# Optimization experiments

Measured on AMD Instinct MI355X. Metric: run time of the kernel, lower is better.

The kernel has to match this reference:

```python
import jax, jax.numpy as jnp
import numpy as np

N_NODES = 100000


def gcn_conv(x, edge_index, W, b):
    """PyG GCNConv: add self-loops, symmetric deg^{-1/2} normalization,
    linear transform, scatter-add aggregation, then bias."""
    n = x.shape[0]
    loops = jnp.arange(n, dtype=edge_index.dtype)
    src = jnp.concatenate([edge_index[0], loops])  # [E+N]
    dst = jnp.concatenate([edge_index[1], loops])  # [E+N]
    # degree (with self-loops) of each target node
    deg = jax.ops.segment_sum(jnp.ones_like(dst, dtype=x.dtype), dst, num_segments=n)
    dinv = jnp.where(deg > 0, jax.lax.rsqrt(deg), 0.0)
    norm = dinv[src] * dinv[dst]  # [E+N]
    h = x @ W  # [N, out_dim] -- transform before aggregation
    msg = h[src] * norm[:, None]  # gather + normalize
    out = jax.ops.segment_sum(msg, dst, num_segments=n)  # scatter-add
    return out + b


def setup_inputs() -> dict:
    key = jax.random.key(0)
    ks = jax.random.split(key, 8)
    n, e, d_in, d_h = N_NODES, 1600000, 32, 64
    x = jax.random.normal(ks[0], (n, d_in), dtype=jnp.float32)
    edge_index = jax.random.randint(ks[1], (2, e), 0, n, dtype=jnp.int64)
    # Glorot-style init for GCN weights, uniform for linear layer
    W1 = jax.random.normal(ks[2], (d_in, d_h), dtype=jnp.float32) / np.sqrt(d_in)
    b1 = jnp.zeros((d_h,), dtype=jnp.float32)
    W2 = jax.random.normal(ks[3], (d_h, d_h), dtype=jnp.float32) / np.sqrt(d_h)
    b2 = jnp.zeros((d_h,), dtype=jnp.float32)
    Wo = jax.random.normal(ks[4], (d_h, 1), dtype=jnp.float32) / np.sqrt(d_h)
    bo = jnp.zeros((1,), dtype=jnp.float32)
    return {"x": x, "edge_index": edge_index, "W1": W1, "b1": b1,
            "W2": W2, "b2": b2, "Wo": Wo, "bo": bo}


def reference(x, edge_index, W1, b1, W2, b2, Wo, bo):
    h = jax.nn.relu(gcn_conv(x, edge_index, W1, b1))
    h = jax.nn.relu(gcn_conv(h, edge_index, W2, b2))
    logits = h @ Wo + bo  # [N, 1]
    return jax.nn.sigmoid(logits).squeeze(-1)  # [N]
```

## Files before the change

kernel.cpp:

```cpp
#include <hip/hip_runtime.h>

#define DH 64
#define DIN 32
#define BSH 8
#define BNODES 256
#define MAXB 1024
#define CAPSH 13
#define CAP (1 << CAPSH)

typedef unsigned short u16;
typedef unsigned int u32;
typedef float f32x2 __attribute__((ext_vector_type(2)));

__device__ __forceinline__ float bf2f(u16 u) {
    union { u32 i; float f; } x; x.i = ((u32)u) << 16; return x.f;
}
__device__ __forceinline__ u16 f2bf(float f) {
    union { float f; u32 i; } x; x.f = f;
    u32 r = x.i + 0x7fff + ((x.i >> 16) & 1);
    return (u16)(r >> 16);
}
__device__ __forceinline__ float bfl(u32 u) {
    union { u32 i; float f; } x; x.i = u << 16; return x.f;
}
__device__ __forceinline__ float bfh(u32 u) {
    union { u32 i; float f; } x; x.i = u & 0xffff0000u; return x.f;
}
__device__ __forceinline__ void pkacc(f32x2& a, u32 u) {
    f32x2 b;
    b[0] = bfl(u); b[1] = bfh(u);
    asm("v_pk_add_f32 %0, %1, %0" : "+v"(a) : "v"(b));
}

__global__ void __launch_bounds__(1024) binA_k(
        const int* __restrict__ ei, int* __restrict__ gcnt,
        u32* __restrict__ pairs, int E, int n, int nbuck) {
    __shared__ int lhist[MAXB];
    __shared__ int lbase[MAXB];
    __shared__ int smode;
    int t = threadIdx.x;
    if (t < 64) {
        int v = (2 * t + 1 < 2 * E) ? ei[2 * t + 1] : 0;
        unsigned long long b = __ballot(v != 0);
        if (t == 0) smode = (b != 0ULL) ? 1 : 0;
    }
    for (int b = t; b < nbuck; b += 1024) lhist[b] = 0;
    __syncthreads();
    int m = smode;
    unsigned un = (unsigned)n;
    int q0 = blockIdx.x * 1024 + t;
    int qs = gridDim.x * 1024;

    if (m && !(E & 3)) {
        const int4* d4 = (const int4*)(ei + E);
        for (int q = q0; q < (E >> 2); q += qs) {
            int4 d = d4[q];
            if ((unsigned)d.x < un) atomicAdd(&lhist[d.x >> BSH], 1);
            if ((unsigned)d.y < un) atomicAdd(&lhist[d.y >> BSH], 1);
            if ((unsigned)d.z < un) atomicAdd(&lhist[d.z >> BSH], 1);
            if ((unsigned)d.w < un) atomicAdd(&lhist[d.w >> BSH], 1);
        }
    } else if (!m && !(E & 1)) {
        const int4* d4 = (const int4*)(ei + 2 * E);
        for (int q = q0; q < (E >> 1); q += qs) {
            int4 d = d4[q];
            if ((unsigned)d.x < un) atomicAdd(&lhist[d.x >> BSH], 1);
            if ((unsigned)d.z < un) atomicAdd(&lhist[d.z >> BSH], 1);
        }
    } else {
        const int* dstp = m ? (ei + E) : (ei + 2 * E);
        int stride = m ? 1 : 2;
        for (int e = q0; e < E; e += qs) {
            int d = dstp[(size_t)e * stride];
            if ((unsigned)d < un) atomicAdd(&lhist[d >> BSH], 1);
        }
    }
    __syncthreads();
    for (int b = t; b < nbuck; b += 1024) {
        int c = lhist[b];
        lbase[b] = c ? ((b << CAPSH) + atomicAdd(&gcnt[b], c)) : 0;
        lhist[b] = 0;
    }
    __syncthreads();
    #define EMIT(S, D)                                                     \
        if ((unsigned)(D) < un) {                                          \
            int sv = ((unsigned)(S) < un) ? (S) : 0;                       \
            int bb = (D) >> BSH;                                           \
            int off = atomicAdd(&lhist[bb], 1);                            \
            int pos = lbase[bb] + off;                                     \
            if (pos < ((bb + 1) << CAPSH))                                 \
                pairs[pos] = ((u32)sv << BSH) | (u32)((D) & (BNODES - 1)); \
        }
    if (m && !(E & 3)) {
        const int4* s4 = (const int4*)ei;
        const int4* d4 = (const int4*)(ei + E);
        for (int q = q0; q < (E >> 2); q += qs) {
            int4 s = s4[q]; int4 d = d4[q];
            EMIT(s.x, d.x) EMIT(s.y, d.y) EMIT(s.z, d.z) EMIT(s.w, d.w)
        }
    } else if (!m && !(E & 1)) {
        const int4* s4 = (const int4*)ei;
        const int4* d4 = (const int4*)(ei + 2 * E);
        for (int q = q0; q < (E >> 1); q += qs) {
            int4 s = s4[q]; int4 d = d4[q];
            EMIT(s.x, d.x) EMIT(s.z, d.z)
        }
    } else {
        const int* srcp = ei;
        const int* dstp = m ? (ei + E) : (ei + 2 * E);
        int stride = m ? 1 : 2;
        for (int e = q0; e < E; e += qs) {
            int d = dstp[(size_t)e * stride];
            int s = srcp[(size_t)e * stride];
            EMIT(s, d)
        }
    }
    #undef EMIT
}

__global__ void __launch_bounds__(1024) csr_build_k(
        const u32* __restrict__ pairs, const int* __restrict__ gcnt,
        int2* __restrict__ rse,
        int* __restrict__ col, float* __restrict__ dinv, int N) {
    __shared__ int cnt[BNODES];
    __shared__ int s[BNODES];
    int b = blockIdx.x, t = threadIdx.x;
    int base = b << CAPSH;
    int ec = gcnt[b]; if (ec > CAP) ec = CAP;
    int end = base + ec;
    if (t < BNODES) cnt[t] = 0;
    __syncthreads();
    for (int i = base + t; i < end; i += 1024)
        atomicAdd(&cnt[pairs[i] & (BNODES - 1)], 1);
    __syncthreads();
    int v = (t < BNODES) ? cnt[t] : 0;
    if (t < BNODES) s[t] = v;
    __syncthreads();
    for (int off = 1; off < BNODES; off <<= 1) {
        int xsc = (t >= off && t < BNODES) ? s[t - off] : 0;
        __syncthreads();
        if (t < BNODES) s[t] += xsc;
        __syncthreads();
    }
    if (t < BNODES) {
        int excl = s[t] - v;
        int a = base + excl;
        int node = (b << BSH) + t;
        if (node < N) {
            rse[node]  = make_int2(a, a + v);
            dinv[node] = rsqrtf((float)v + 1.0f);
        }
        cnt[t] = a;
    }
    __syncthreads();
    for (int i = base + t; i < end; i += 1024) {
        u32 p = pairs[i];
        int pos = atomicAdd(&cnt[p & (BNODES - 1)], 1);
        col[pos] = (int)((p >> BSH) << 7);
    }
}

__global__ void __launch_bounds__(256) gemm1_k(
        const float* __restrict__ x, const float* __restrict__ W1,
        const float* __restrict__ dinv, u16* __restrict__ hp, int N) {
    __shared__ float Wl[DIN * DH];
    __shared__ float xl[16][DIN + 4];
    int t = threadIdx.x;
    {
        const float4* Wv = (const float4*)W1;
        float4* Wd = (float4*)Wl;
        #pragma unroll
        for (int r = 0; r < 2; r++) Wd[t + 256 * r] = Wv[t + 256 * r];
    }
    if (blockIdx.x == 0 && t < 32)
        ((float*)(hp + (size_t)N * DH))[t] = 0.f;
    if (t < 128) {
        int row = t >> 3, ck = (t & 7) * 4;
        int node = blockIdx.x * 16 + row;
        float4 vx = {0.f, 0.f, 0.f, 0.f};
        if (node < N)
            vx = *(const float4*)&x[(size_t)node * DIN + ck];
        *(float4*)&xl[row][ck] = vx;
    }
    __syncthreads();
    int lane = t & 63, w = t >> 6;
    int g = lane >> 4, c = lane & 15;
    int nl = w * 4 + g;
    int node = blockIdx.x * 16 + nl;
    const float* xr = xl[nl];
    float4 acc = {0.f, 0.f, 0.f, 0.f};
    #pragma unroll
    for (int k = 0; k < DIN; k++) {
        float xv = xr[k];
        float4 wv = *(const float4*)&Wl[k * DH + c * 4];
        acc.x += xv * wv.x; acc.y += xv * wv.y; acc.z += xv * wv.z; acc.w += xv * wv.w;
    }
    if (node < N) {
        float di = dinv[node];
        ushort4 o;
        o.x = f2bf(acc.x * di); o.y = f2bf(acc.y * di);
        o.z = f2bf(acc.z * di); o.w = f2bf(acc.w * di);
        *(ushort4*)&hp[(size_t)node * DH + c * 4] = o;
    }
}

__device__ __forceinline__ void edge_sum_roll8(const u16* __restrict__ hp,
                                               const int* __restrict__ colb,
                                               int start, int deg, int gl, int c,
                                               int sentb, f32x2* __restrict__ acc) {
    int dm = deg;
    dm = max(dm, __shfl_xor(dm, 8, 64));
    dm = max(dm, __shfl_xor(dm, 16, 64));
    dm = max(dm, __shfl_xor(dm, 32, 64));
    if (dm <= 0) return;
    const char* hpco = (const char*)hp + ((u32)c << 4);
    int nch = (dm + 7) >> 3;
    uint4 v0, v1, v2, v3, v4, v5, v6, v7;
    int cb = (c < deg) ? colb[start + c] : sentb;
    {
        int s;
        s = __shfl(cb, gl | 0, 64); v0 = *(const uint4*)(hpco + s);
        s = __shfl(cb, gl | 1, 64); v1 = *(const uint4*)(hpco + s);
        s = __shfl(cb, gl | 2, 64); v2 = *(const uint4*)(hpco + s);
        s = __shfl(cb, gl | 3, 64); v3 = *(const uint4*)(hpco + s);
        s = __shfl(cb, gl | 4, 64); v4 = *(const uint4*)(hpco + s);
        s = __shfl(cb, gl | 5, 64); v5 = *(const uint4*)(hpco + s);
        s = __shfl(cb, gl | 6, 64); v6 = *(const uint4*)(hpco + s);
        s = __shfl(cb, gl | 7, 64); v7 = *(const uint4*)(hpco + s);
    }
    int cbn = (8 + c < deg) ? colb[start + 8 + c] : sentb;
    for (int ch = 1; ch < nch; ch++) {
        int cbu = cbn;
        int nb2 = (ch + 1) << 3;
        cbn = (nb2 + c < deg) ? colb[start + nb2 + c] : sentb;
        int s;
        s = __shfl(cbu, gl | 0, 64);
        pkacc(acc[0], v0.x); pkacc(acc[1], v0.y); pkacc(acc[2], v0.z); pkacc(acc[3], v0.w);
        v0 = *(const uint4*)(hpco + s);
        s = __shfl(cbu, gl | 1, 64);
        pkacc(acc[0], v1.x); pkacc(acc[1], v1.y); pkacc(acc[2], v1.z); pkacc(acc[3], v1.w);
        v1 = *(const uint4*)(hpco + s);
        s = __shfl(cbu, gl | 2, 64);
        pkacc(acc[0], v2.x); pkacc(acc[1], v2.y); pkacc(acc[2], v2.z); pkacc(acc[3], v2.w);
        v2 = *(const uint4*)(hpco + s);
        s = __shfl(cbu, gl | 3, 64);
        pkacc(acc[0], v3.x); pkacc(acc[1], v3.y); pkacc(acc[2], v3.z); pkacc(acc[3], v3.w);
        v3 = *(const uint4*)(hpco + s);
        s = __shfl(cbu, gl | 4, 64);
        pkacc(acc[0], v4.x); pkacc(acc[1], v4.y); pkacc(acc[2], v4.z); pkacc(acc[3], v4.w);
        v4 = *(const uint4*)(hpco + s);
        s = __shfl(cbu, gl | 5, 64);
        pkacc(acc[0], v5.x); pkacc(acc[1], v5.y); pkacc(acc[2], v5.z); pkacc(acc[3], v5.w);
        v5 = *(const uint4*)(hpco + s);
        s = __shfl(cbu, gl | 6, 64);
        pkacc(acc[0], v6.x); pkacc(acc[1], v6.y); pkacc(acc[2], v6.z); pkacc(acc[3], v6.w);
        v6 = *(const uint4*)(hpco + s);
        s = __shfl(cbu, gl | 7, 64);
        pkacc(acc[0], v7.x); pkacc(acc[1], v7.y); pkacc(acc[2], v7.z); pkacc(acc[3], v7.w);
        v7 = *(const uint4*)(hpco + s);
    }
    pkacc(acc[0], v0.x); pkacc(acc[1], v0.y); pkacc(acc[2], v0.z); pkacc(acc[3], v0.w);
    pkacc(acc[0], v1.x); pkacc(acc[1], v1.y); pkacc(acc[2], v1.z); pkacc(acc[3], v1.w);
    pkacc(acc[0], v2.x); pkacc(acc[1], v2.y); pkacc(acc[2], v2.z); pkacc(acc[3], v2.w);
    pkacc(acc[0], v3.x); pkacc(acc[1], v3.y); pkacc(acc[2], v3.z); pkacc(acc[3], v3.w);
    pkacc(acc[0], v4.x); pkacc(acc[1], v4.y); pkacc(acc[2], v4.z); pkacc(acc[3], v4.w);
    pkacc(acc[0], v5.x); pkacc(acc[1], v5.y); pkacc(acc[2], v5.z); pkacc(acc[3], v5.w);
    pkacc(acc[0], v6.x); pkacc(acc[1], v6.y); pkacc(acc[2], v6.z); pkacc(acc[3], v6.w);
    pkacc(acc[0], v7.x); pkacc(acc[1], v7.y); pkacc(acc[2], v7.z); pkacc(acc[3], v7.w);
}

__global__ void __launch_bounds__(256) agg_gemm_k(
        const u16* __restrict__ hp, const int2* __restrict__ rse,
        const int* __restrict__ col,
        const float* __restrict__ dinv, const float* __restrict__ b1,
        const float* __restrict__ W2, u16* __restrict__ hp2, int N) {
    __shared__ float Wl[DH * DH];
    __shared__ float xs[4][8][DH + 4];
    int tid = threadIdx.x;
    {
        const float4* Wv = (const float4*)W2;
        float4* Wd = (float4*)Wl;
        #pragma unroll
        for (int r = 0; r < 4; r++) Wd[tid + 256 * r] = Wv[tid + 256 * r];
    }
    if (blockIdx.x == 0 && tid < 32)
        ((float*)(hp2 + (size_t)N * DH))[tid] = 0.f;
    __syncthreads();
    int lane = tid & 63, w = tid >> 6;
    int g = lane >> 3, c = lane & 7, gl = g << 3;
    int node = blockIdx.x * 32 + w * 8 + g;
    int start = 0, deg = 0;
    if (node < N) { int2 se = rse[node]; start = se.x; deg = se.y - se.x; }
    f32x2 acc[4] = {{0.f,0.f},{0.f,0.f},{0.f,0.f},{0.f,0.f}};
    edge_sum_roll8(hp, col, start, deg, gl, c, N << 7, acc);
    float di = (node < N) ? dinv[node] : 0.f;
    float o0=0.f,o1=0.f,o2=0.f,o3=0.f,o4=0.f,o5=0.f,o6=0.f,o7=0.f;
    if (node < N) {
        uint4 sv = *(const uint4*)&hp[(size_t)node * DH + c * 8];
        float4 blo = *(const float4*)&b1[c * 8];
        float4 bhi = *(const float4*)&b1[c * 8 + 4];
        o0 = fmaxf((acc[0][0] + bfl(sv.x)) * di + blo.x, 0.f);
        o1 = fmaxf((acc[0][1] + bfh(sv.x)) * di + blo.y, 0.f);
        o2 = fmaxf((acc[1][0] + bfl(sv.y)) * di + blo.z, 0.f);
        o3 = fmaxf((acc[1][1] + bfh(sv.y)) * di + blo.w, 0.f);
        o4 = fmaxf((acc[2][0] + bfl(sv.z)) * di + bhi.x, 0.f);
        o5 = fmaxf((acc[2][1] + bfh(sv.z)) * di + bhi.y, 0.f);
        o6 = fmaxf((acc[3][0] + bfl(sv.w)) * di + bhi.z, 0.f);
        o7 = fmaxf((acc[3][1] + bfh(sv.w)) * di + bhi.w, 0.f);
    }
    *(float4*)&xs[w][g][c * 8]     = make_float4(o0, o1, o2, o3);
    *(float4*)&xs[w][g][c * 8 + 4] = make_float4(o4, o5, o6, o7);
    const float* xr = xs[w][g];
    float4 alo = {0.f,0.f,0.f,0.f}, ahi = {0.f,0.f,0.f,0.f};
    #pragma unroll
    for (int k4 = 0; k4 < DH / 4; k4++) {
        float4 xv4 = *(const float4*)&xr[k4 * 4];
        float xj[4] = {xv4.x, xv4.y, xv4.z, xv4.w};
        #pragma unroll
        for (int j = 0; j < 4; j++) {
            const float* wr = &Wl[(k4 * 4 + j) * DH + c * 8];
            float4 w0 = *(const float4*)wr;
            float4 w1 = *(const float4*)(wr + 4);
            float xv = xj[j];
            alo.x += xv * w0.x; alo.y += xv * w0.y; alo.z += xv * w0.z; alo.w += xv * w0.w;
            ahi.x += xv * w1.x; ahi.y += xv * w1.y; ahi.z += xv * w1.z; ahi.w += xv * w1.w;
        }
    }
    if (node < N) {
        uint4 po;
        po.x = (u32)f2bf(alo.x * di) | ((u32)f2bf(alo.y * di) << 16);
        po.y = (u32)f2bf(alo.z * di) | ((u32)f2bf(alo.w * di) << 16);
        po.z = (u32)f2bf(ahi.x * di) | ((u32)f2bf(ahi.y * di) << 16);
        po.w = (u32)f2bf(ahi.z * di) | ((u32)f2bf(ahi.w * di) << 16);
        *(uint4*)&hp2[(size_t)node * DH + c * 8] = po;
    }
}

__global__ void __launch_bounds__(256) agg_head_k(
        const u16* __restrict__ hp, const int2* __restrict__ rse,
        const int* __restrict__ col,
        const float* __restrict__ dinv, const float* __restrict__ bias,
        const float* __restrict__ Wo, const float* __restrict__ bo,
        float* __restrict__ y, int N) {
    int lane = threadIdx.x & 63;
    int g = lane >> 3, c = lane & 7, gl = g << 3;
    int node = blockIdx.x * 32 + (threadIdx.x >> 6) * 8 + g;
    int start = 0, deg = 0;
    if (node < N) { int2 se = rse[node]; start = se.x; deg = se.y - se.x; }
    f32x2 acc[4] = {{0.f,0.f},{0.f,0.f},{0.f,0.f},{0.f,0.f}};
    edge_sum_roll8(hp, col, start, deg, gl, c, N << 7, acc);
    float t = 0.f;
    if (node < N) {
        uint4 sv = *(const uint4*)&hp[(size_t)node * DH + c * 8];
        float4 blo = *(const float4*)&bias[c * 8];
        float4 bhi = *(const float4*)&bias[c * 8 + 4];
        float4 wlo = *(const float4*)&Wo[c * 8];
        float4 whi = *(const float4*)&Wo[c * 8 + 4];
        float di = dinv[node];
        t = fmaxf((acc[0][0] + bfl(sv.x)) * di + blo.x, 0.f) * wlo.x
          + fmaxf((acc[0][1] + bfh(sv.x)) * di + blo.y, 0.f) * wlo.y
          + fmaxf((acc[1][0] + bfl(sv.y)) * di + blo.z, 0.f) * wlo.z
          + fmaxf((acc[1][1] + bfh(sv.y)) * di + blo.w, 0.f) * wlo.w
          + fmaxf((acc[2][0] + bfl(sv.z)) * di + bhi.x, 0.f) * whi.x
          + fmaxf((acc[2][1] + bfh(sv.z)) * di + bhi.y, 0.f) * whi.y
          + fmaxf((acc[3][0] + bfl(sv.w)) * di + bhi.z, 0.f) * whi.z
          + fmaxf((acc[3][1] + bfh(sv.w)) * di + bhi.w, 0.f) * whi.w;
    }
    t += __shfl_xor(t, 1, 64);
    t += __shfl_xor(t, 2, 64);
    t += __shfl_xor(t, 4, 64);
    if (c == 0 && node < N) {
        float z = t + bo[0];
        y[node] = 1.f / (1.f + __expf(-z));
    }
}

extern "C" void kernel_launch(void* const* d_in, const int* in_sizes, int n_in,
                              void* d_out, int out_size, void* d_ws, size_t ws_size,
                              hipStream_t stream) {
    const float* x  = (const float*)d_in[0];
    const int*   ei = (const int*)d_in[1];
    const float* W1 = (const float*)d_in[2];
    const float* b1 = (const float*)d_in[3];
    const float* W2 = (const float*)d_in[4];
    const float* b2 = (const float*)d_in[5];
    const float* Wo = (const float*)d_in[6];
    const float* bo = (const float*)d_in[7];
    float* y = (float*)d_out;

    int N = in_sizes[0] / DIN;
    int E = in_sizes[1] / 2;
    int nbuck = ((N - 1) >> BSH) + 1;

    char* ws = (char*)d_ws;
    size_t off = 0;
    auto alloc = [&](size_t bytes) { char* p = ws + off; off += (bytes + 255) & ~(size_t)255; return p; };
    int*   gcnt   = (int*)alloc(MAXB * 4);
    int2*  rse    = (int2*)alloc((size_t)N * 8);
    float* dinv   = (float*)alloc((size_t)N * 4);
    int*   col    = (int*)alloc(((size_t)nbuck << CAPSH) * 4);
    size_t pair_b = ((size_t)nbuck << CAPSH) * 4;
    size_t hp_b   = (size_t)N * DH * 2 + 256;
    char*  bufA   = (char*)alloc(pair_b > hp_b ? pair_b : hp_b);
    u16*   bufB   = (u16*)alloc(hp_b);
    u16*   hp    = (u16*)bufA;
    u32*   pairs = (u32*)bufA;

    hipMemsetAsync(gcnt, 0, (size_t)nbuck * 4, stream);
    binA_k<<<256, 1024, 0, stream>>>(ei, gcnt, pairs, E, N, nbuck);
    csr_build_k<<<nbuck, 1024, 0, stream>>>(pairs, gcnt, rse, col, dinv, N);
    gemm1_k<<<(N + 15) / 16, 256, 0, stream>>>(x, W1, dinv, hp, N);
    agg_gemm_k<<<(N + 31) / 32, 256, 0, stream>>>(hp, rse, col, dinv, b1, W2, bufB, N);
    agg_head_k<<<(N + 31) / 32, 256, 0, stream>>>(bufB, rse, col, dinv, b2, Wo, bo, y, N);
}
```

Before: 182.3 us.

## Sort nodes by degree so aggregation wavefronts process similar-degree nodes

Adds a degree histogram in csr_build_k and a new dscat_k kernel that counting-sorts node ids by clamped degree into nmap. Both aggregation kernels then map each 8-lane group to nmap[idx] instead of the contiguous node id. This aims to reduce load imbalance in the edge loops of a wavefront, since each wavefront waits on its highest-degree node. The cost is an extra kernel launch, global atomics on 64 counters, and scattered writes for outputs and self-feature reads because consecutive groups no longer touch neighbouring nodes.

```diff
diff --git a/kernel.cpp b/kernel.cpp
--- a/kernel.cpp
+++ b/kernel.cpp
@@ -121,7 +121,8 @@
 __global__ void __launch_bounds__(1024) csr_build_k(
         const u32* __restrict__ pairs, const int* __restrict__ gcnt,
         int2* __restrict__ rse,
-        int* __restrict__ col, float* __restrict__ dinv, int N) {
+        int* __restrict__ col, float* __restrict__ dinv,
+        int* __restrict__ dhist, int N) {
     __shared__ int cnt[BNODES];
     __shared__ int s[BNODES];
     int b = blockIdx.x, t = threadIdx.x;
@@ -149,6 +150,7 @@
         if (node < N) {
             rse[node]  = make_int2(a, a + v);
             dinv[node] = rsqrtf((float)v + 1.0f);
+            atomicAdd(&dhist[v > 63 ? 63 : v], 1);
         }
         cnt[t] = a;
     }
@@ -157,6 +159,30 @@
         u32 p = pairs[i];
         int pos = atomicAdd(&cnt[p & (BNODES - 1)], 1);
         col[pos] = (int)((p >> BSH) << 7);
+    }
+}
+
+__global__ void __launch_bounds__(256) dscat_k(
+        const int2* __restrict__ rse, const int* __restrict__ dhist,
+        int* __restrict__ dcnt2, int* __restrict__ nmap, int N) {
+    __shared__ int dbase[64];
+    int t = threadIdx.x;
+    if (t < 64) {
+        int v = dhist[t];
+        int x = v;
+        for (int off = 1; off < 64; off <<= 1) {
+            int y = __shfl_up(x, off, 64);
+            if (t >= off) x += y;
+        }
+        dbase[t] = x - v;
+    }
+    __syncthreads();
+    int i = blockIdx.x * 256 + t;
+    if (i < N) {
+        int2 se = rse[i];
+        int d = se.y - se.x; if (d > 63) d = 63;
+        int pos = dbase[d] + atomicAdd(&dcnt2[d], 1);
+        nmap[pos] = i;
     }
 }
 
@@ -271,7 +297,7 @@
 
 __global__ void __launch_bounds__(256) agg_gemm_k(
         const u16* __restrict__ hp, const int2* __restrict__ rse,
-        const int* __restrict__ col,
+        const int* __restrict__ col, const int* __restrict__ nmap,
         const float* __restrict__ dinv, const float* __restrict__ b1,
         const float* __restrict__ W2, u16* __restrict__ hp2, int N) {
     __shared__ float Wl[DH * DH];
@@ -288,7 +314,8 @@
     __syncthreads();
     int lane = tid & 63, w = tid >> 6;
     int g = lane >> 3, c = lane & 7, gl = g << 3;
-    int node = blockIdx.x * 32 + w * 8 + g;
+    int idx = blockIdx.x * 32 + w * 8 + g;
+    int node = (idx < N) ? nmap[idx] : N;
     int start = 0, deg = 0;
     if (node < N) { int2 se = rse[node]; start = se.x; deg = se.y - se.x; }
     f32x2 acc[4] = {{0.f,0.f},{0.f,0.f},{0.f,0.f},{0.f,0.f}};
@@ -338,13 +365,14 @@
 
 __global__ void __launch_bounds__(256) agg_head_k(
         const u16* __restrict__ hp, const int2* __restrict__ rse,
-        const int* __restrict__ col,
+        const int* __restrict__ col, const int* __restrict__ nmap,
         const float* __restrict__ dinv, const float* __restrict__ bias,
         const float* __restrict__ Wo, const float* __restrict__ bo,
         float* __restrict__ y, int N) {
     int lane = threadIdx.x & 63;
     int g = lane >> 3, c = lane & 7, gl = g << 3;
-    int node = blockIdx.x * 32 + (threadIdx.x >> 6) * 8 + g;
+    int idx = blockIdx.x * 32 + (threadIdx.x >> 6) * 8 + g;
+    int node = (idx < N) ? nmap[idx] : N;
     int start = 0, deg = 0;
     if (node < N) { int2 se = rse[node]; start = se.x; deg = se.y - se.x; }
     f32x2 acc[4] = {{0.f,0.f},{0.f,0.f},{0.f,0.f},{0.f,0.f}};
@@ -395,9 +423,12 @@
     char* ws = (char*)d_ws;
     size_t off = 0;
     auto alloc = [&](size_t bytes) { char* p = ws + off; off += (bytes + 255) & ~(size_t)255; return p; };
-    int*   gcnt   = (int*)alloc(MAXB * 4);
+    int*   gcnt   = (int*)alloc((MAXB + 128) * 4);
+    int*   dhist  = gcnt + MAXB;
+    int*   dcnt2  = gcnt + MAXB + 64;
     int2*  rse    = (int2*)alloc((size_t)N * 8);
     float* dinv   = (float*)alloc((size_t)N * 4);
+    int*   nmap   = (int*)alloc((size_t)N * 4);
     int*   col    = (int*)alloc(((size_t)nbuck << CAPSH) * 4);
     size_t pair_b = ((size_t)nbuck << CAPSH) * 4;
     size_t hp_b   = (size_t)N * DH * 2 + 256;
@@ -406,10 +437,11 @@
     u16*   hp    = (u16*)bufA;
     u32*   pairs = (u32*)bufA;
 
-    hipMemsetAsync(gcnt, 0, (size_t)nbuck * 4, stream);
+    hipMemsetAsync(gcnt, 0, (size_t)(MAXB + 128) * 4, stream);
     binA_k<<<256, 1024, 0, stream>>>(ei, gcnt, pairs, E, N, nbuck);
-    csr_build_k<<<nbuck, 1024, 0, stream>>>(pairs, gcnt, rse, col, dinv, N);
+    csr_build_k<<<nbuck, 1024, 0, stream>>>(pairs, gcnt, rse, col, dinv, dhist, N);
+    dscat_k<<<(N + 255) / 256, 256, 0, stream>>>(rse, dhist, dcnt2, nmap, N);
     gemm1_k<<<(N + 15) / 16, 256, 0, stream>>>(x, W1, dinv, hp, N);
-    agg_gemm_k<<<(N + 31) / 32, 256, 0, stream>>>(hp, rse, col, dinv, b1, W2, bufB, N);
-    agg_head_k<<<(N + 31) / 32, 256, 0, stream>>>(bufB, rse, col, dinv, b2, Wo, bo, y, N);
-}
+    agg_gemm_k<<<(N + 31) / 32, 256, 0, stream>>>(hp, rse, col, nmap, dinv, b1, W2, bufB, N);
+    agg_head_k<<<(N + 31) / 32, 256, 0, stream>>>(bufB, rse, col, nmap, dinv, b2, Wo, bo, y, N);
+}
```

Result: slower. 706.7 us (+287.6%).
